# Optimization experiments

Hardware: AMD Instinct MI355X
Metric: run time of the kernel (lower is better)

The kernel has to match this reference:

```python
import jax, jax.numpy as jnp
import numpy as np

B, T, DIM, H = 32, 1024, 512, 8
HD = DIM // H
HID = int(DIM * 4.0)
EPS = 1e-6
SCALE = HD ** -0.5


def _ln(t, g, b):
    m = t.mean(-1, keepdims=True)
    var = ((t - m) ** 2).mean(-1, keepdims=True)
    return (t - m) * jax.lax.rsqrt(var + EPS) * g + b


def setup_inputs() -> dict:
    key = jax.random.key(0)
    ks = jax.random.split(key, 10)
    n = lambda k, s: jax.random.normal(k, s, dtype=jnp.float32)
    w = lambda k, s: n(k, s) * 0.02
    z = lambda d: jnp.zeros((d,), dtype=jnp.float32)
    o = lambda d: jnp.ones((d,), dtype=jnp.float32)
    return {
        'x': n(ks[0], (B, T, DIM)),
        'k': n(ks[1], (T, H, B, HD)),
        'v': n(ks[2], (T, H, B, HD)),
        'Wqkv': w(ks[3], (DIM, 3 * DIM)), 'bqkv': z(3 * DIM),
        'Wsa': w(ks[4], (DIM, DIM)), 'bsa': z(DIM),
        'Wq': w(ks[5], (DIM, DIM)), 'bq': z(DIM),
        'Wed': w(ks[6], (DIM, DIM)), 'bed': z(DIM),
        'g1': o(DIM), 'be1': z(DIM),
        'g2': o(DIM), 'be2': z(DIM),
        'g3': o(DIM), 'be3': z(DIM),
        'W1': w(ks[7], (DIM, HID)), 'b1': z(HID),
        'W2': w(ks[8], (HID, DIM)), 'b2': z(DIM),
    }


def _decoder_block(x, k, v, Wqkv, bqkv, Wsa, bsa, Wq, bq, Wed, bed,
                   g1, be1, g2, be2, g3, be3, W1, b1, W2, b2):
    # ---- self-attention (faithful to the original, degenerate einsums) ----
    qkv = x @ Wqkv + bqkv                                        # [B,T,3*DIM]
    qkv = qkv.reshape(B, T, 3, H, HD).transpose(2, 1, 3, 0, 4)   # [3,T,H,B,HD]
    q, sk, sv = qkv[0], qkv[1], qkv[2]
    dp = jnp.einsum('kabc,qdef->qabe', sk, q) * SCALE            # [T,H,B,B]
    scores = jax.nn.softmax(dp, axis=-1)
    wa = jnp.einsum('qabc,kdef->bqaf', scores, sv).reshape(B, T, DIM)
    attn = wa @ Wsa + bsa
    an1 = _ln(attn + x, g1, be1)
    # ---- encoder-decoder attention ----
    qe = (an1 @ Wq + bq).reshape(B, T, H, HD).transpose(1, 2, 0, 3)  # [T,H,B,HD]
    dp2 = jnp.einsum('abkd,abqd->abqk', k, qe) * SCALE           # [T,H,B,B]
    sc2 = jax.nn.softmax(dp2, axis=-1)
    wa2 = jnp.einsum('abts,abse->tabe', sc2, v).reshape(B, T, DIM)
    attn2 = wa2 @ Wed + bed
    an2 = _ln(attn2 + x, g2, be2)
    # ---- MLP (exact GELU, as nn.GELU default) ----
    hmid = jax.nn.gelu(an2 @ W1 + b1, approximate=False)
    z = hmid @ W2 + b2
    return _ln(z + an2, g3, be3)


def reference(x, k, v, Wqkv, bqkv, Wsa, bsa, Wq, bq, Wed, bed,
              g1, be1, g2, be2, g3, be3, W1, b1, W2, b2):
    return _decoder_block(x, k, v, Wqkv, bqkv, Wsa, bsa, Wq, bq, Wed, bed,
                          g1, be1, g2, be2, g3, be3, W1, b1, W2, b2)
```

## Files before the change

### kernel.cpp

```cpp
#include <hip/hip_runtime.h>
#include <hip/hip_bf16.h>
#include <math.h>

#define Bn 32
#define Tn 1024
#define DIMn 512
#define Hn 8
#define HDn 64
#define HIDn 2048
#define Mn 32768

using short8 = __attribute__((ext_vector_type(8))) short;
using half8  = __attribute__((ext_vector_type(8))) _Float16;
using f32x4  = __attribute__((ext_vector_type(4))) float;
typedef unsigned short u16;
typedef unsigned int   u32;

__device__ __forceinline__ u16 f2h(float x) {
  _Float16 h = (_Float16)x;
  return __builtin_bit_cast(u16, h);
}
__device__ __forceinline__ float h2f(u16 u) {
  return (float)__builtin_bit_cast(_Float16, u);
}
__device__ __forceinline__ u32 pack2h(float a, float b) {
  return (u32)f2h(a) | ((u32)f2h(b) << 16);
}
__device__ __forceinline__ void gld16(const void* g, void* l) {
  __builtin_amdgcn_global_load_lds((const __attribute__((address_space(1))) u32*)g,
                                   (__attribute__((address_space(3))) u32*)l, 16, 0, 0);
}
__device__ __forceinline__ float wredsum(float v) {
  #pragma unroll
  for (int d = 1; d < 64; d <<= 1) v += __shfl_xor(v, d, 64);
  return v;
}
__device__ __forceinline__ void hard_barrier() {
  asm volatile("" ::: "memory");
  __builtin_amdgcn_s_barrier();
  asm volatile("" ::: "memory");
}
__device__ __forceinline__ float fast_gelu(float v) {
  const float ax = fabsf(v) * 0.70710678118654752f;
  const float t = 1.0f / (1.0f + 0.3275911f * ax);
  const float p = ((((1.061405429f * t - 1.453152027f) * t) + 1.421413741f) * t - 0.284496736f) * t + 0.254829592f;
  const float y = 1.0f - p * t * __expf(-ax * ax);
  const float erfv = (v >= 0.f) ? y : -y;
  return 0.5f * v * (1.0f + erfv);
}

__global__ __launch_bounds__(256) void colsum1(const float* __restrict__ x, float* __restrict__ part) {
  const int b = blockIdx.x, t = threadIdx.x;
  const float* p = x + (size_t)b * 128 * DIMn;
  float a0 = 0.f, a1 = 0.f;
  for (int r = 0; r < 128; ++r) {
    a0 += p[r * DIMn + t];
    a1 += p[r * DIMn + t + 256];
  }
  part[b * DIMn + t] = a0;
  part[b * DIMn + t + 256] = a1;
}

__global__ __launch_bounds__(256) void colsum2(const float* __restrict__ part, float* __restrict__ xs) {
  const int c = blockIdx.x * 256 + threadIdx.x;
  float a = 0.f;
  for (int b = 0; b < 256; ++b) a += part[b * DIMn + c];
  xs[c] = a;
}

__global__ __launch_bounds__(256) void sv_k(const float* __restrict__ xs, const float* __restrict__ Wqkv,
                                            const float* __restrict__ bqkv, float* __restrict__ SVp) {
  __shared__ float xsh[512];
  __shared__ float red[4][64];
  const int h = blockIdx.x, q = threadIdx.x >> 6, f = threadIdx.x & 63;
  xsh[threadIdx.x] = xs[threadIdx.x];
  xsh[threadIdx.x + 256] = xs[threadIdx.x + 256];
  __syncthreads();
  const int colb = 2 * DIMn + h * HDn + f;
  float acc = 0.f;
  for (int i = q * 128; i < q * 128 + 128; ++i) acc += xsh[i] * Wqkv[(size_t)i * 1536 + colb];
  red[q][f] = acc;
  __syncthreads();
  if (q == 0)
    SVp[h * 64 + f] = red[0][f] + red[1][f] + red[2][f] + red[3][f] + 32768.0f * bqkv[colb];
}

__global__ __launch_bounds__(256) void attnc2_k(const float* __restrict__ SVp, const float* __restrict__ Wsa,
                                                const float* __restrict__ bsa, float* __restrict__ attnc) {
  __shared__ float SVs[64];
  __shared__ float red[4][64];
  const int q = threadIdx.x >> 6, jj = threadIdx.x & 63;
  if (threadIdx.x < 64) {
    float s = 0.f;
    #pragma unroll
    for (int h = 0; h < 8; ++h) s += SVp[h * 64 + threadIdx.x];
    SVs[threadIdx.x] = s;
  }
  __syncthreads();
  const int j = blockIdx.x * 64 + jj;
  float acc = 0.f;
  for (int i = q * 128; i < q * 128 + 128; ++i) acc += SVs[i & 63] * Wsa[(size_t)i * DIMn + j];
  red[q][jj] = acc;
  __syncthreads();
  if (q == 0) attnc[j] = red[0][jj] + red[1][jj] + red[2][jj] + red[3][jj] + bsa[j];
}

__global__ __launch_bounds__(256) void wtrans(const float* __restrict__ W, u16* __restrict__ WT, int K, int N) {
  __shared__ float tile[64][65];
  const int n0 = blockIdx.x * 64, k0 = blockIdx.y * 64;
  const int t = threadIdx.x;
  #pragma unroll
  for (int i = 0; i < 16; ++i) {
    const int fl = i * 256 + t, r = fl >> 6, c = fl & 63;
    tile[r][c] = W[(size_t)(k0 + r) * N + n0 + c];
  }
  __syncthreads();
  #pragma unroll
  for (int i = 0; i < 16; ++i) {
    const int fl = i * 256 + t, r = fl >> 6, c = fl & 63;
    WT[(size_t)(n0 + r) * K + k0 + c] = f2h(tile[c][r]);
  }
}

template <int MODE>
__global__ __launch_bounds__(256) void ln_k(const void* __restrict__ Ap, const void* __restrict__ Bp,
                                            const float* __restrict__ cv, const float* __restrict__ g,
                                            const float* __restrict__ be, void* __restrict__ outp) {
  const int row = blockIdx.x * 4 + (threadIdx.x >> 6);
  const int l = threadIdx.x & 63;
  const size_t base = (size_t)row * DIMn + l * 8;
  float v[8];
  if (MODE == 0 || MODE == 2) {
    const float* a = (const float*)Ap + base;
    float4 x0 = *(const float4*)a;
    float4 x1 = *(const float4*)(a + 4);
    v[0] = x0.x; v[1] = x0.y; v[2] = x0.z; v[3] = x0.w;
    v[4] = x1.x; v[5] = x1.y; v[6] = x1.z; v[7] = x1.w;
  } else {
    short8 s = *(const short8*)((const u16*)Ap + base);
    #pragma unroll
    for (int i = 0; i < 8; ++i) v[i] = h2f((u16)s[i]);
  }
  if (MODE == 0) {
    float4 c0 = *(const float4*)(cv + l * 8);
    float4 c1 = *(const float4*)(cv + l * 8 + 4);
    v[0] += c0.x; v[1] += c0.y; v[2] += c0.z; v[3] += c0.w;
    v[4] += c1.x; v[5] += c1.y; v[6] += c1.z; v[7] += c1.w;
  } else if (MODE == 1) {
    const float* b = (const float*)Bp + base;
    float4 x0 = *(const float4*)b;
    float4 x1 = *(const float4*)(b + 4);
    v[0] += x0.x; v[1] += x0.y; v[2] += x0.z; v[3] += x0.w;
    v[4] += x1.x; v[5] += x1.y; v[6] += x1.z; v[7] += x1.w;
  } else {
    short8 s2 = *(const short8*)((const u16*)Bp + base);
    #pragma unroll
    for (int i = 0; i < 8; ++i) v[i] += h2f((u16)s2[i]);
  }
  float s = 0.f;
  #pragma unroll
  for (int i = 0; i < 8; ++i) s += v[i];
  s = wredsum(s);
  const float mean = s * (1.0f / 512.0f);
  float q = 0.f;
  #pragma unroll
  for (int i = 0; i < 8; ++i) { const float d = v[i] - mean; q += d * d; }
  q = wredsum(q);
  const float rs = rsqrtf(q * (1.0f / 512.0f) + 1e-6f);
  float gg[8], bb[8];
  {
    float4 g0 = *(const float4*)(g + l * 8);
    float4 g1 = *(const float4*)(g + l * 8 + 4);
    float4 b0 = *(const float4*)(be + l * 8);
    float4 b1 = *(const float4*)(be + l * 8 + 4);
    gg[0] = g0.x; gg[1] = g0.y; gg[2] = g0.z; gg[3] = g0.w;
    gg[4] = g1.x; gg[5] = g1.y; gg[6] = g1.z; gg[7] = g1.w;
    bb[0] = b0.x; bb[1] = b0.y; bb[2] = b0.z; bb[3] = b0.w;
    bb[4] = b1.x; bb[5] = b1.y; bb[6] = b1.z; bb[7] = b1.w;
  }
  float y[8];
  #pragma unroll
  for (int i = 0; i < 8; ++i) y[i] = (v[i] - mean) * rs * gg[i] + bb[i];
  if (MODE == 2) {
    float* o = (float*)outp + base;
    *(float4*)o = make_float4(y[0], y[1], y[2], y[3]);
    *(float4*)(o + 4) = make_float4(y[4], y[5], y[6], y[7]);
  } else {
    short8 o;
    #pragma unroll
    for (int i = 0; i < 8; ++i) o[i] = (short)f2h(y[i]);
    *(short8*)((u16*)outp + base) = o;
  }
}

#define CROW 272
template <bool GELU, bool OBF>
__global__ __launch_bounds__(512) void gemm_bt(const u16* __restrict__ A, const u16* __restrict__ BT,
                                               const float* __restrict__ bias, u16* __restrict__ OB,
                                               float* __restrict__ OF, int Ni, int Ki, int gridX) {
  __shared__ u16 smem[49152];
  const int tid = threadIdx.x;
  const int l = tid & 63, wid = tid >> 6, wr = wid >> 2, wc = wid & 3;

  int wg = blockIdx.x;
  const int nwg = gridDim.x;
  if ((nwg & 7) == 0) {
    const int q = nwg >> 3;
    wg = (wg & 7) * q + (wg >> 3);
  }
  const int bx = wg % gridX, by = wg / gridX;
  const int m0 = by * 256, n0 = bx * 256;
  const int r16 = l & 15, g4 = l >> 4;

  const int srow = tid >> 2, schunk = (tid & 3) * 8;
  const u16* gaA = A  + (size_t)(m0 + srow) * (size_t)Ki + schunk;
  const u16* gaB = BT + (size_t)(n0 + srow) * (size_t)Ki + schunk;
  const size_t rowskip = (size_t)128 * (size_t)Ki;
  const int ldst = tid * 8;

  int aoff[8], boff[4];
  #pragma unroll
  for (int mi = 0; mi < 8; ++mi) aoff[mi] = (wr * 128 + mi * 16 + r16) * 32 + g4 * 8;
  #pragma unroll
  for (int ni = 0; ni < 4; ++ni) boff[ni] = 8192 + (wc * 64 + ni * 16 + r16) * 32 + g4 * 8;

  f32x4 acc[8][4] = {};
  const int nt = Ki >> 5;

  auto STAGE = [&](int t, int b) {
    u16* base = smem + b * 16384;
    const int kk = t * 32;
    gld16(gaA + kk, &base[ldst]);
    gld16(gaA + kk + rowskip, &base[ldst + 4096]);
    gld16(gaB + kk, &base[8192 + ldst]);
    gld16(gaB + kk + rowskip, &base[8192 + ldst + 4096]);
  };

  STAGE(0, 0);
  STAGE(1, 1);
  int b0 = 0, b1 = 1, b2 = 2;
  for (int t = 0; t < nt; ++t) {
    if (t < nt - 1) asm volatile("s_waitcnt vmcnt(4)" ::: "memory");
    else            asm volatile("s_waitcnt vmcnt(0)" ::: "memory");
    hard_barrier();
    if (t + 2 < nt) STAGE(t + 2, b2);
    const u16* base = smem + b0 * 16384;
    half8 bf[4];
    #pragma unroll
    for (int ni = 0; ni < 4; ++ni) bf[ni] = *(const half8*)&base[boff[ni]];
    #pragma unroll
    for (int mi = 0; mi < 8; ++mi) {
      half8 af = *(const half8*)&base[aoff[mi]];
      #pragma unroll
      for (int ni = 0; ni < 4; ++ni)
        acc[mi][ni] = __builtin_amdgcn_mfma_f32_16x16x32_f16(af, bf[ni], acc[mi][ni], 0, 0, 0);
    }
    hard_barrier();
    const int tb = b0; b0 = b1; b1 = b2; b2 = tb;
  }

  if (OBF) {
    u16* Cs = smem;
    float bv[4];
    #pragma unroll
    for (int ni = 0; ni < 4; ++ni) bv[ni] = bias[n0 + wc * 64 + ni * 16 + r16];
    #pragma unroll
    for (int p = 0; p < 2; ++p) {
      #pragma unroll
      for (int mi4 = 0; mi4 < 4; ++mi4) {
        const int mi = p * 4 + mi4;
        #pragma unroll
        for (int ni = 0; ni < 4; ++ni) {
          const int colL = wc * 64 + ni * 16 + r16;
          #pragma unroll
          for (int r = 0; r < 4; ++r) {
            float v = acc[mi][ni][r] + bv[ni];
            if (GELU) v = fast_gelu(v);
            Cs[wr * (64 * CROW) + (mi4 * 16 + g4 * 4 + r) * CROW + colL] = f2h(v);
          }
        }
      }
      hard_barrier();
      #pragma unroll
      for (int j = 0; j < 8; ++j) {
        const int s = tid + j * 512;
        const int wrS = s >> 11;
        const int rowL = (s & 2047) >> 5;
        const int c8 = s & 31;
        *(short8*)(OB + (size_t)(m0 + wrS * 128 + p * 64 + rowL) * Ni + n0 + c8 * 8) =
            *(const short8*)&Cs[wrS * (64 * CROW) + rowL * CROW + c8 * 8];
      }
      if (p == 0) hard_barrier();
    }
  } else {
    #pragma unroll
    for (int ni = 0; ni < 4; ++ni) {
      const int col = n0 + wc * 64 + ni * 16 + r16;
      const float bvv = bias[col];
      #pragma unroll
      for (int mi = 0; mi < 8; ++mi) {
        const int rowb = m0 + wr * 128 + mi * 16 + g4 * 4;
        #pragma unroll
        for (int r = 0; r < 4; ++r) {
          float v = acc[mi][ni][r] + bvv;
          if (GELU) v = fast_gelu(v);
          OF[(size_t)(rowb + r) * Ni + col] = v;
        }
      }
    }
  }
}

__global__ __launch_bounds__(64) void attn_k(const u16* __restrict__ qe, const float* __restrict__ kin,
                                             const float* __restrict__ vin, u16* __restrict__ wa2) {
  const int t = blockIdx.x >> 3;
  const int h = blockIdx.x & 7;
  const int l = threadIdx.x;
  __shared__ u16 Kq[32 * 80];
  __shared__ u16 Qq[32 * 80];
  __shared__ u16 VT[64 * 48];
  __shared__ u16 Ps[32 * 48];

  const float* kp = kin + (size_t)blockIdx.x * 2048;
  const float* vp = vin + (size_t)blockIdx.x * 2048;
  #pragma unroll
  for (int i = 0; i < 8; ++i) {
    const int fl = i * 256 + l * 4;
    const int r = fl >> 6, c = fl & 63;
    float4 kv = *(const float4*)(kp + fl);
    float4 vv = *(const float4*)(vp + fl);
    *(u32*)&Kq[r * 80 + c]     = pack2h(kv.x, kv.y);
    *(u32*)&Kq[r * 80 + c + 2] = pack2h(kv.z, kv.w);
    VT[(c + 0) * 48 + r] = f2h(vv.x);
    VT[(c + 1) * 48 + r] = f2h(vv.y);
    VT[(c + 2) * 48 + r] = f2h(vv.z);
    VT[(c + 3) * 48 + r] = f2h(vv.w);
  }
  {
    const int qb = l >> 1, hf = l & 1;
    const u16* qp = qe + (size_t)(qb * Tn + t) * DIMn + h * HDn + hf * 32;
    #pragma unroll
    for (int j = 0; j < 4; ++j) {
      short8 d = *(const short8*)(qp + j * 8);
      *(short8*)&Qq[qb * 80 + hf * 32 + j * 8] = d;
    }
  }
  __syncthreads();

  const int r16 = l & 15, g4 = l >> 4;
  f32x4 sacc[2][2] = {};
  #pragma unroll
  for (int kk = 0; kk < 2; ++kk) {
    half8 aQ0 = *(const half8*)&Qq[r16 * 80 + kk * 32 + g4 * 8];
    half8 aQ1 = *(const half8*)&Qq[(16 + r16) * 80 + kk * 32 + g4 * 8];
    half8 bK0 = *(const half8*)&Kq[r16 * 80 + kk * 32 + g4 * 8];
    half8 bK1 = *(const half8*)&Kq[(16 + r16) * 80 + kk * 32 + g4 * 8];
    sacc[0][0] = __builtin_amdgcn_mfma_f32_16x16x32_f16(aQ0, bK0, sacc[0][0], 0, 0, 0);
    sacc[0][1] = __builtin_amdgcn_mfma_f32_16x16x32_f16(aQ0, bK1, sacc[0][1], 0, 0, 0);
    sacc[1][0] = __builtin_amdgcn_mfma_f32_16x16x32_f16(aQ1, bK0, sacc[1][0], 0, 0, 0);
    sacc[1][1] = __builtin_amdgcn_mfma_f32_16x16x32_f16(aQ1, bK1, sacc[1][1], 0, 0, 0);
  }
  #pragma unroll
  for (int m = 0; m < 2; ++m) {
    #pragma unroll
    for (int r = 0; r < 4; ++r) {
      const float a0 = sacc[m][0][r] * 0.125f;
      const float a1 = sacc[m][1][r] * 0.125f;
      float mx = fmaxf(a0, a1);
      #pragma unroll
      for (int d = 1; d < 16; d <<= 1) mx = fmaxf(mx, __shfl_xor(mx, d, 64));
      const float e0 = __expf(a0 - mx), e1 = __expf(a1 - mx);
      float sm = e0 + e1;
      #pragma unroll
      for (int d = 1; d < 16; d <<= 1) sm += __shfl_xor(sm, d, 64);
      const float inv = 1.0f / sm;
      const int rr = m * 16 + g4 * 4 + r;
      Ps[rr * 48 + r16]      = f2h(e0 * inv);
      Ps[rr * 48 + 16 + r16] = f2h(e1 * inv);
    }
  }
  __syncthreads();

  half8 aP0 = *(const half8*)&Ps[r16 * 48 + g4 * 8];
  half8 aP1 = *(const half8*)&Ps[(16 + r16) * 48 + g4 * 8];
  f32x4 oacc[2][4] = {};
  #pragma unroll
  for (int nn = 0; nn < 4; ++nn) {
    half8 bV = *(const half8*)&VT[(nn * 16 + r16) * 48 + g4 * 8];
    oacc[0][nn] = __builtin_amdgcn_mfma_f32_16x16x32_f16(aP0, bV, oacc[0][nn], 0, 0, 0);
    oacc[1][nn] = __builtin_amdgcn_mfma_f32_16x16x32_f16(aP1, bV, oacc[1][nn], 0, 0, 0);
  }
  #pragma unroll
  for (int m = 0; m < 2; ++m) {
    #pragma unroll
    for (int r = 0; r < 4; ++r) {
      const int qb = m * 16 + g4 * 4 + r;
      u16* op = wa2 + (size_t)(qb * Tn + t) * DIMn + h * HDn;
      #pragma unroll
      for (int nn = 0; nn < 4; ++nn)
        op[nn * 16 + r16] = f2h(oacc[m][nn][r]);
    }
  }
}

extern "C" void kernel_launch(void* const* d_in, const int* in_sizes, int n_in,
                              void* d_out, int out_size, void* d_ws, size_t ws_size,
                              hipStream_t stream) {
  (void)in_sizes; (void)n_in; (void)out_size;
  const float* x    = (const float*)d_in[0];
  const float* kin  = (const float*)d_in[1];
  const float* vin  = (const float*)d_in[2];
  const float* Wqkv = (const float*)d_in[3];
  const float* bqkv = (const float*)d_in[4];
  const float* Wsa  = (const float*)d_in[5];
  const float* bsa  = (const float*)d_in[6];
  const float* Wq   = (const float*)d_in[7];
  const float* bq   = (const float*)d_in[8];
  const float* Wed  = (const float*)d_in[9];
  const float* bed  = (const float*)d_in[10];
  const float* g1   = (const float*)d_in[11];
  const float* be1  = (const float*)d_in[12];
  const float* g2   = (const float*)d_in[13];
  const float* be2  = (const float*)d_in[14];
  const float* g3   = (const float*)d_in[15];
  const float* be3  = (const float*)d_in[16];
  const float* W1   = (const float*)d_in[17];
  const float* b1   = (const float*)d_in[18];
  const float* W2   = (const float*)d_in[19];
  const float* b2   = (const float*)d_in[20];

  char* ws = (char*)d_ws;
  float* xs    = (float*)(ws);
  float* SVp   = (float*)(ws + (2 << 10));
  float* attnc = (float*)(ws + (4 << 10));
  float* part  = (float*)(ws + (6 << 10));
  u16* wqT  = (u16*)(ws + (1 << 20));
  u16* wedT = (u16*)(ws + (1 << 20) + (512 << 10));
  u16* w1T  = (u16*)(ws + (2 << 20));
  u16* w2T  = (u16*)(ws + (4 << 20));
  u16* Abuf = (u16*)(ws + (6 << 20));
  const size_t HOFF = 38ull << 20;
  u16* hmid = (u16*)(ws + HOFF);

  u16* an1  = Abuf;
  u16* wa2  = Abuf;
  u16* an2b = Abuf;
  u16*   qe   = (u16*)d_out;
  u16*   a2bf = (u16*)d_out;
  float* zf   = (float*)d_out;

  long long avail = (long long)ws_size - (long long)HOFF;
  int crows = (avail > 0) ? (int)(avail / (HIDn * 2)) : 256;
  crows = (crows / 256) * 256;
  if (crows < 256) crows = 256;
  if (crows > Mn) crows = Mn;

  colsum1<<<256, 256, 0, stream>>>(x, part);
  colsum2<<<2, 256, 0, stream>>>(part, xs);
  sv_k<<<8, 256, 0, stream>>>(xs, Wqkv, bqkv, SVp);
  attnc2_k<<<8, 256, 0, stream>>>(SVp, Wsa, bsa, attnc);

  wtrans<<<dim3(8, 8),  256, 0, stream>>>(Wq,  wqT,  512, 512);
  wtrans<<<dim3(8, 8),  256, 0, stream>>>(Wed, wedT, 512, 512);
  wtrans<<<dim3(32, 8), 256, 0, stream>>>(W1,  w1T,  512, 2048);
  wtrans<<<dim3(8, 32), 256, 0, stream>>>(W2,  w2T,  2048, 512);

  ln_k<0><<<Mn / 4, 256, 0, stream>>>(x, nullptr, attnc, g1, be1, an1);
  gemm_bt<false, true><<<256, 512, 0, stream>>>(an1, wqT, bq, qe, nullptr, 512, 512, 2);
  attn_k<<<Tn * Hn, 64, 0, stream>>>(qe, kin, vin, wa2);
  gemm_bt<false, true><<<256, 512, 0, stream>>>(wa2, wedT, bed, a2bf, nullptr, 512, 512, 2);
  ln_k<1><<<Mn / 4, 256, 0, stream>>>(a2bf, x, nullptr, g2, be2, an2b);
  for (int r0 = 0; r0 < Mn; r0 += crows) {
    int rc = Mn - r0; if (rc > crows) rc = crows;
    gemm_bt<true, true><<<8 * (rc / 256), 512, 0, stream>>>(an2b + (size_t)r0 * DIMn, w1T, b1, hmid, nullptr, HIDn, DIMn, 8);
    gemm_bt<false, false><<<2 * (rc / 256), 512, 0, stream>>>(hmid, w2T, b2, nullptr, zf + (size_t)r0 * DIMn, DIMn, HIDn, 2);
  }
  ln_k<2><<<Mn / 4, 256, 0, stream>>>(zf, an2b, nullptr, g3, be3, d_out);
}
```

Baseline: 414.7 us.

## Add 128x128 triple-buffered GEMM kernel for the MLP up-projection

Introduces a new 128x128-tile GEMM with 256 threads, three LDS stages and an XOR-swizzled shared-memory layout. It is used only for the W1 up-projection with GELU, and the old 256x256 kernel is renamed and kept for the other GEMMs. The aim is more workgroups and better latency hiding from deeper pipelining on the K=512 GEMM. The cost is lower data reuse per tile, which means more global and LDS traffic per FLOP.

```diff
diff --git a/kernel.cpp b/kernel.cpp
--- a/kernel.cpp
+++ b/kernel.cpp
@@ -193,9 +193,119 @@
   }
 }
 
+#define CPAD 132
+template <bool GELU, bool OBF>
+__global__ __launch_bounds__(256) void gemm128(const u16* __restrict__ A, const u16* __restrict__ BT,
+                                               const float* __restrict__ bias, u16* __restrict__ OB,
+                                               float* __restrict__ OF, int Ni, int Ki, int gridX) {
+  __shared__ u16 smem[3 * 8192];
+  const int tid = threadIdx.x;
+  const int l = tid & 63, w = tid >> 6, wr = w >> 1, wc = w & 1;
+
+  int wg = blockIdx.x;
+  const int nwg = gridDim.x;
+  if ((nwg & 7) == 0) {
+    const int q = nwg >> 3;
+    wg = (wg & 7) * q + (wg >> 3);
+  }
+  const int bx = wg % gridX, by = wg / gridX;
+  const int m0 = by * 128, n0 = bx * 128;
+  const int r16 = l & 15, g4 = l >> 4;
+
+  const int schunk = (tid & 3) ^ ((tid >> 2) & 3);
+  const u16* ga = A + (size_t)(m0 + (tid >> 2)) * (size_t)Ki + schunk * 8;
+  const u16* gb = BT + (size_t)(n0 + (tid >> 2)) * (size_t)Ki + schunk * 8;
+  const int ldst = tid * 8;
+
+  const int g4s = g4 ^ (r16 & 3);
+  int aoff[4], boff[4];
+  #pragma unroll
+  for (int i = 0; i < 4; ++i) {
+    aoff[i] = (wr * 64 + i * 16 + r16) * 32 + g4s * 8;
+    boff[i] = 4096 + (wc * 64 + i * 16 + r16) * 32 + g4s * 8;
+  }
+  f32x4 acc[4][4] = {};
+
+  const int nt = Ki >> 5;
+  auto STAGE = [&](int t, int b) {
+    u16* base = smem + b * 8192;
+    const int kk = t * 32;
+    gld16(ga + kk, &base[ldst]);
+    gld16(ga + kk + (size_t)64 * Ki, &base[ldst + 2048]);
+    gld16(gb + kk, &base[4096 + ldst]);
+    gld16(gb + kk + (size_t)64 * Ki, &base[4096 + ldst + 2048]);
+  };
+
+  STAGE(0, 0);
+  STAGE(1, 1);
+  int b0 = 0, b1 = 1, b2 = 2;
+  for (int t = 0; t < nt; ++t) {
+    if (t < nt - 1) asm volatile("s_waitcnt vmcnt(4)" ::: "memory");
+    else            asm volatile("s_waitcnt vmcnt(0)" ::: "memory");
+    hard_barrier();
+    if (t + 2 < nt) STAGE(t + 2, b2);
+    const u16* base = smem + b0 * 8192;
+    half8 af[4], bf[4];
+    #pragma unroll
+    for (int i = 0; i < 4; ++i) af[i] = *(const half8*)&base[aoff[i]];
+    #pragma unroll
+    for (int i = 0; i < 4; ++i) bf[i] = *(const half8*)&base[boff[i]];
+    #pragma unroll
+    for (int mi = 0; mi < 4; ++mi)
+      #pragma unroll
+      for (int ni = 0; ni < 4; ++ni)
+        acc[mi][ni] = __builtin_amdgcn_mfma_f32_16x16x32_f16(af[mi], bf[ni], acc[mi][ni], 0, 0, 0);
+    hard_barrier();
+    const int tb = b0; b0 = b1; b1 = b2; b2 = tb;
+  }
+
+  if (OBF) {
+    u16* Cs = smem;
+    #pragma unroll
+    for (int ni = 0; ni < 4; ++ni) {
+      const int col = wc * 64 + ni * 16 + r16;
+      const float bv = bias[n0 + col];
+      #pragma unroll
+      for (int mi = 0; mi < 4; ++mi) {
+        const int rowb = wr * 64 + mi * 16 + g4 * 4;
+        #pragma unroll
+        for (int r = 0; r < 4; ++r) {
+          float v = acc[mi][ni][r] + bv;
+          if (GELU) v = fast_gelu(v);
+          Cs[(rowb + r) * CPAD + col] = f2h(v);
+        }
+      }
+    }
+    hard_barrier();
+    const int rr = tid >> 4;
+    const int c0 = (tid & 15) * 8;
+    #pragma unroll
+    for (int j = 0; j < 8; ++j) {
+      const int row = rr + j * 16;
+      *(short8*)(OB + (size_t)(m0 + row) * Ni + n0 + c0) = *(const short8*)&Cs[row * CPAD + c0];
+    }
+  } else {
+    #pragma unroll
+    for (int ni = 0; ni < 4; ++ni) {
+      const int col = n0 + wc * 64 + ni * 16 + r16;
+      const float bv = bias[col];
+      #pragma unroll
+      for (int mi = 0; mi < 4; ++mi) {
+        const int rowb = m0 + wr * 64 + mi * 16 + g4 * 4;
+        #pragma unroll
+        for (int r = 0; r < 4; ++r) {
+          float v = acc[mi][ni][r] + bv;
+          if (GELU) v = fast_gelu(v);
+          OF[(size_t)(rowb + r) * Ni + col] = v;
+        }
+      }
+    }
+  }
+}
+
 #define CROW 272
 template <bool GELU, bool OBF>
-__global__ __launch_bounds__(512) void gemm_bt(const u16* __restrict__ A, const u16* __restrict__ BT,
+__global__ __launch_bounds__(512) void gemm256(const u16* __restrict__ A, const u16* __restrict__ BT,
                                                const float* __restrict__ bias, u16* __restrict__ OB,
                                                float* __restrict__ OF, int Ni, int Ki, int gridX) {
   __shared__ u16 smem[49152];
@@ -466,14 +576,14 @@
   wtrans<<<dim3(8, 32), 256, 0, stream>>>(W2,  w2T,  2048, 512);
 
   ln_k<0><<<Mn / 4, 256, 0, stream>>>(x, nullptr, attnc, g1, be1, an1);
-  gemm_bt<false, true><<<256, 512, 0, stream>>>(an1, wqT, bq, qe, nullptr, 512, 512, 2);
+  gemm256<false, true><<<256, 512, 0, stream>>>(an1, wqT, bq, qe, nullptr, 512, 512, 2);
   attn_k<<<Tn * Hn, 64, 0, stream>>>(qe, kin, vin, wa2);
-  gemm_bt<false, true><<<256, 512, 0, stream>>>(wa2, wedT, bed, a2bf, nullptr, 512, 512, 2);
+  gemm256<false, true><<<256, 512, 0, stream>>>(wa2, wedT, bed, a2bf, nullptr, 512, 512, 2);
   ln_k<1><<<Mn / 4, 256, 0, stream>>>(a2bf, x, nullptr, g2, be2, an2b);
   for (int r0 = 0; r0 < Mn; r0 += crows) {
     int rc = Mn - r0; if (rc > crows) rc = crows;
-    gemm_bt<true, true><<<8 * (rc / 256), 512, 0, stream>>>(an2b + (size_t)r0 * DIMn, w1T, b1, hmid, nullptr, HIDn, DIMn, 8);
-    gemm_bt<false, false><<<2 * (rc / 256), 512, 0, stream>>>(hmid, w2T, b2, nullptr, zf + (size_t)r0 * DIMn, DIMn, HIDn, 2);
+    gemm128<true, true><<<16 * (rc / 128), 256, 0, stream>>>(an2b + (size_t)r0 * DIMn, w1T, b1, hmid, nullptr, HIDn, DIMn, 16);
+    gemm256<false, false><<<2 * (rc / 256), 512, 0, stream>>>(hmid, w2T, b2, nullptr, zf + (size_t)r0 * DIMn, DIMn, HIDn, 2);
   }
   ln_k<2><<<Mn / 4, 256, 0, stream>>>(zf, an2b, nullptr, g3, be3, d_out);
 }
```

Result: faster. 405.0 us (-2.3%).

## Rewrite GEMM main loop with K=64 tiles, XOR-swizzled LDS, and phased prefetch

Applied to the files above, without the earlier changes.

The GEMM kernel moves from a triple-buffered K=32 tile pipeline to a double-buffered K=64 pipeline. Each K tile is split into four phases that interleave LDS fragment reads, global-to-LDS prefetch of the next tile, and MFMA bursts wrapped in s_setprio. LDS columns are XOR-swizzled by row to avoid bank conflicts on the wider rows. The aim is fewer barriers per K and better overlap of loads with MFMAs. The cost is 128KB of LDS per block instead of 96KB, plus extra barriers inside each tile.

```diff
diff --git a/kernel.cpp b/kernel.cpp
--- a/kernel.cpp
+++ b/kernel.cpp
@@ -195,10 +195,10 @@
 
 #define CROW 272
 template <bool GELU, bool OBF>
-__global__ __launch_bounds__(512) void gemm_bt(const u16* __restrict__ A, const u16* __restrict__ BT,
-                                               const float* __restrict__ bias, u16* __restrict__ OB,
-                                               float* __restrict__ OF, int Ni, int Ki, int gridX) {
-  __shared__ u16 smem[49152];
+__global__ __launch_bounds__(512) void gemm8p(const u16* __restrict__ A, const u16* __restrict__ BT,
+                                              const float* __restrict__ bias, u16* __restrict__ OB,
+                                              float* __restrict__ OF, int Ni, int Ki, int gridX) {
+  __shared__ u16 smem[65536];
   const int tid = threadIdx.x;
   const int l = tid & 63, wid = tid >> 6, wr = wid >> 2, wc = wid & 3;
 
@@ -212,51 +212,81 @@
   const int m0 = by * 256, n0 = bx * 256;
   const int r16 = l & 15, g4 = l >> 4;
 
-  const int srow = tid >> 2, schunk = (tid & 3) * 8;
-  const u16* gaA = A  + (size_t)(m0 + srow) * (size_t)Ki + schunk;
-  const u16* gaB = BT + (size_t)(n0 + srow) * (size_t)Ki + schunk;
-  const size_t rowskip = (size_t)128 * (size_t)Ki;
-  const int ldst = tid * 8;
-
-  int aoff[8], boff[4];
-  #pragma unroll
-  for (int mi = 0; mi < 8; ++mi) aoff[mi] = (wr * 128 + mi * 16 + r16) * 32 + g4 * 8;
-  #pragma unroll
-  for (int ni = 0; ni < 4; ++ni) boff[ni] = 8192 + (wc * 64 + ni * 16 + r16) * 32 + g4 * 8;
+  const int srow = tid >> 3;
+  const int schunk8 = ((tid & 7) ^ (srow & 7)) * 8;
+  const u16* gA = A  + (size_t)(m0 + srow) * (size_t)Ki + schunk8;
+  const u16* gB = BT + (size_t)(n0 + srow) * (size_t)Ki + schunk8;
+  const size_t r64 = (size_t)64 * Ki, r128 = (size_t)128 * Ki, r192 = (size_t)192 * Ki;
+  const int ld = tid * 8;
+
+  const int c0 = (g4 ^ (r16 & 7)) * 8;
+  const int c1 = ((4 + g4) ^ (r16 & 7)) * 8;
 
   f32x4 acc[8][4] = {};
-  const int nt = Ki >> 5;
-
-  auto STAGE = [&](int t, int b) {
-    u16* base = smem + b * 16384;
-    const int kk = t * 32;
-    gld16(gaA + kk, &base[ldst]);
-    gld16(gaA + kk + rowskip, &base[ldst + 4096]);
-    gld16(gaB + kk, &base[8192 + ldst]);
-    gld16(gaB + kk + rowskip, &base[8192 + ldst + 4096]);
-  };
-
-  STAGE(0, 0);
-  STAGE(1, 1);
-  int b0 = 0, b1 = 1, b2 = 2;
-  for (int t = 0; t < nt; ++t) {
-    if (t < nt - 1) asm volatile("s_waitcnt vmcnt(4)" ::: "memory");
-    else            asm volatile("s_waitcnt vmcnt(0)" ::: "memory");
-    hard_barrier();
-    if (t + 2 < nt) STAGE(t + 2, b2);
-    const u16* base = smem + b0 * 16384;
-    half8 bf[4];
-    #pragma unroll
-    for (int ni = 0; ni < 4; ++ni) bf[ni] = *(const half8*)&base[boff[ni]];
-    #pragma unroll
-    for (int mi = 0; mi < 8; ++mi) {
-      half8 af = *(const half8*)&base[aoff[mi]];
-      #pragma unroll
-      for (int ni = 0; ni < 4; ++ni)
-        acc[mi][ni] = __builtin_amdgcn_mfma_f32_16x16x32_f16(af, bf[ni], acc[mi][ni], 0, 0, 0);
+  const int NT = Ki >> 6;
+
+  gld16(gA, &smem[ld]);
+  gld16(gA + r64, &smem[4096 + ld]);
+  gld16(gB, &smem[16384 + ld]);
+  gld16(gB + r64, &smem[20480 + ld]);
+  gld16(gA + r128, &smem[8192 + ld]);
+  gld16(gA + r192, &smem[12288 + ld]);
+  gld16(gB + r128, &smem[24576 + ld]);
+  gld16(gB + r192, &smem[28672 + ld]);
+  asm volatile("s_waitcnt vmcnt(0)" ::: "memory");
+  hard_barrier();
+
+  for (int kt = 0; kt < NT; ++kt) {
+    const int b = kt & 1;
+    const u16* base = smem + b * 32768;
+    u16* nb = smem + (b ^ 1) * 32768;
+    const int nk = (kt + 1) * 64;
+    half8 bf[4][2];
+    #pragma unroll
+    for (int q = 0; q < 4; ++q) {
+      half8 af[2][2];
+      #pragma unroll
+      for (int m2 = 0; m2 < 2; ++m2) {
+        const int ao = (wr * 128 + (q * 2 + m2) * 16 + r16) * 64;
+        af[m2][0] = *(const half8*)&base[ao + c0];
+        af[m2][1] = *(const half8*)&base[ao + c1];
+      }
+      if (q == 0) {
+        #pragma unroll
+        for (int ni = 0; ni < 4; ++ni) {
+          const int bo = 16384 + (wc * 64 + ni * 16 + r16) * 64;
+          bf[ni][0] = *(const half8*)&base[bo + c0];
+          bf[ni][1] = *(const half8*)&base[bo + c1];
+        }
+      }
+      if (kt + 1 < NT) {
+        if (q == 0) {
+          gld16(gA + nk, &nb[ld]);
+          gld16(gA + nk + r64, &nb[4096 + ld]);
+          gld16(gB + nk, &nb[16384 + ld]);
+          gld16(gB + nk + r64, &nb[20480 + ld]);
+        } else if (q == 1) {
+          gld16(gA + nk + r128, &nb[8192 + ld]);
+          gld16(gA + nk + r192, &nb[12288 + ld]);
+          gld16(gB + nk + r128, &nb[24576 + ld]);
+          gld16(gB + nk + r192, &nb[28672 + ld]);
+        }
+      }
+      if (q == 3) asm volatile("s_waitcnt vmcnt(0)" ::: "memory");
+      hard_barrier();
+      asm volatile("s_waitcnt lgkmcnt(0)" ::: "memory");
+      __builtin_amdgcn_sched_barrier(0);
+      __builtin_amdgcn_s_setprio(1);
+      #pragma unroll
+      for (int s = 0; s < 2; ++s)
+        #pragma unroll
+        for (int m2 = 0; m2 < 2; ++m2)
+          #pragma unroll
+          for (int ni = 0; ni < 4; ++ni)
+            acc[q * 2 + m2][ni] = __builtin_amdgcn_mfma_f32_16x16x32_f16(af[m2][s], bf[ni][s], acc[q * 2 + m2][ni], 0, 0, 0);
+      __builtin_amdgcn_s_setprio(0);
+      hard_barrier();
     }
-    hard_barrier();
-    const int tb = b0; b0 = b1; b1 = b2; b2 = tb;
   }
 
   if (OBF) {
@@ -466,14 +496,14 @@
   wtrans<<<dim3(8, 32), 256, 0, stream>>>(W2,  w2T,  2048, 512);
 
   ln_k<0><<<Mn / 4, 256, 0, stream>>>(x, nullptr, attnc, g1, be1, an1);
-  gemm_bt<false, true><<<256, 512, 0, stream>>>(an1, wqT, bq, qe, nullptr, 512, 512, 2);
+  gemm8p<false, true><<<256, 512, 0, stream>>>(an1, wqT, bq, qe, nullptr, 512, 512, 2);
   attn_k<<<Tn * Hn, 64, 0, stream>>>(qe, kin, vin, wa2);
-  gemm_bt<false, true><<<256, 512, 0, stream>>>(wa2, wedT, bed, a2bf, nullptr, 512, 512, 2);
+  gemm8p<false, true><<<256, 512, 0, stream>>>(wa2, wedT, bed, a2bf, nullptr, 512, 512, 2);
   ln_k<1><<<Mn / 4, 256, 0, stream>>>(a2bf, x, nullptr, g2, be2, an2b);
   for (int r0 = 0; r0 < Mn; r0 += crows) {
     int rc = Mn - r0; if (rc > crows) rc = crows;
-    gemm_bt<true, true><<<8 * (rc / 256), 512, 0, stream>>>(an2b + (size_t)r0 * DIMn, w1T, b1, hmid, nullptr, HIDn, DIMn, 8);
-    gemm_bt<false, false><<<2 * (rc / 256), 512, 0, stream>>>(hmid, w2T, b2, nullptr, zf + (size_t)r0 * DIMn, DIMn, HIDn, 2);
+    gemm8p<true, true><<<8 * (rc / 256), 512, 0, stream>>>(an2b + (size_t)r0 * DIMn, w1T, b1, hmid, nullptr, HIDn, DIMn, 8);
+    gemm8p<false, false><<<2 * (rc / 256), 512, 0, stream>>>(hmid, w2T, b2, nullptr, zf + (size_t)r0 * DIMn, DIMn, HIDn, 2);
   }
   ln_k<2><<<Mn / 4, 256, 0, stream>>>(zf, an2b, nullptr, g3, be3, d_out);
 }
```

Result: slower. 424.2 us (+2.3%).
